# Performance work log

Hardware: AMD Instinct MI355X
Metric: run time of the kernel (lower is better)

Reference implementation:

```python
import jax, jax.numpy as jnp
import numpy as np

CHUNK = 128  # chunk size for the chunked causal linear-attention scan
EPS = 1e-6


def _feature_map(x):
    # elu(x) + 1, matching torch.nn.functional.elu (alpha=1)
    return jax.nn.elu(x) + 1.0


def _causal_linear(Q, K, V):
    """Chunked causal linear attention.

    Q, K: [N, H, L, D], V: [N, H, L, Dv] (float32).
    Computes out[l] = Q[l] @ sum_{s<=l} K[s]^T V[s] without materializing
    the O(L*D*Dv) cumulative outer-product tensor.
    """
    N, H, L, D = Q.shape
    Dv = V.shape[-1]
    C = L // CHUNK
    # [C, N, H, T, D]
    qc = jnp.moveaxis(Q.reshape(N, H, C, CHUNK, D), 2, 0)
    kc = jnp.moveaxis(K.reshape(N, H, C, CHUNK, D), 2, 0)
    vc = jnp.moveaxis(V.reshape(N, H, C, CHUNK, Dv), 2, 0)
    tri = jnp.tril(jnp.ones((CHUNK, CHUNK), dtype=Q.dtype))  # causal mask within chunk

    def step(S, qkv):
        q, k, v = qkv  # [N, H, T, D], [N, H, T, D], [N, H, T, Dv]
        attn = jnp.einsum('nhtd,nhsd->nhts', q, k) * tri
        out = jnp.einsum('nhts,nhse->nhte', attn, v) \
            + jnp.einsum('nhtd,nhde->nhte', q, S)
        S = S + jnp.einsum('nhsd,nhse->nhde', k, v)
        return S, out

    S0 = jnp.zeros((N, H, D, Dv), dtype=Q.dtype)
    _, outs = jax.lax.scan(step, S0, (qc, kc, vc))  # outs: [C, N, H, T, Dv]
    return jnp.moveaxis(outs, 0, 2).reshape(N, H, L, Dv)


def setup_inputs() -> dict:
    key = jax.random.key(0)
    kq, kk, kv = jax.random.split(key, 3)
    shape = (4, 8192, 8, 64)  # [N, L, H, D]
    return {
        'queries': jax.random.normal(kq, shape, dtype=jnp.float32),
        'keys': jax.random.normal(kk, shape, dtype=jnp.float32),
        'values': jax.random.normal(kv, shape, dtype=jnp.float32),
    }


def reference(queries, keys, values):
    dtype = queries.dtype
    Q = _feature_map(queries)  # [N, L, H, D]
    K = _feature_map(keys)
    # normalizer: Z = 1 / (Q . cumsum_l(K) + eps), shape [N, L, H]
    Z = 1.0 / (jnp.einsum('nlhi,nlhi->nlh', Q, jnp.cumsum(K, axis=1)) + EPS)
    # numerator computed in float32 per original causal_linear
    Qf = jnp.transpose(Q, (0, 2, 1, 3)).astype(jnp.float32)
    Kf = jnp.transpose(K, (0, 2, 1, 3)).astype(jnp.float32)
    Vf = jnp.transpose(values, (0, 2, 1, 3)).astype(jnp.float32)
    Vn = _causal_linear(Qf, Kf, Vf)  # [N, H, L, Dv]
    Vn = jnp.transpose(Vn, (0, 2, 1, 3)).astype(dtype)  # [N, L, H, Dv]
    return Vn * Z[:, :, :, None]
```

## Files before the change

### kernel.cpp

```cpp
#include <hip/hip_runtime.h>
#include <hip/hip_bf16.h>
#include <math.h>

#define N_    4
#define L_    8192
#define H_    8
#define NH_   32
#define CHK   64
#define NC_   128
#define ROWF  512
#define EPSF  1e-6f

typedef __attribute__((ext_vector_type(8))) short bf16x8;
typedef __attribute__((ext_vector_type(4))) float f32x4;
typedef __attribute__((ext_vector_type(4))) unsigned short us4;

__device__ __forceinline__ float fmap(float x) { return x > 0.f ? x + 1.f : __expf(x); }

__device__ __forceinline__ unsigned short c2bf(float x) {
  __hip_bfloat16 b = __float2bfloat16(x);
  return *reinterpret_cast<unsigned short*>(&b);
}
__device__ __forceinline__ float bf2f(unsigned short u) {
  return __uint_as_float(((unsigned)u) << 16);
}

__device__ __forceinline__ int sidx(int row, int col) {
  return row * 64 + (col ^ ((row & 7) << 3));
}

__device__ __forceinline__ f32x4 MFMA(bf16x8 a, bf16x8 b, f32x4 c) {
  return __builtin_amdgcn_mfma_f32_16x16x32_bf16(a, b, c, 0, 0, 0);
}

__global__ __launch_bounds__(512) void k_chunk_tot(const float* __restrict__ keys,
                                                   const float* __restrict__ values,
                                                   unsigned short* __restrict__ Tws,
                                                   float* __restrict__ Kcs) {
  __shared__ __align__(16) unsigned short Kt[64 * 64];
  __shared__ __align__(16) unsigned short Vt[64 * 64];
  __shared__ float kacc[64];
  const int bid = blockIdx.x;
  const int nh = bid / NC_, c = bid % NC_;
  const int n = nh / H_, h = nh % H_;
  const int tid = threadIdx.x;
  const int lane = tid & 63;
  const int wv = tid >> 6;
  const int lane15 = lane & 15, lg = lane >> 4;
  const int arow = (wv & 3) * 16 + lane15;
  const int nt0 = (wv >> 2) * 2;

  if (tid < 64) kacc[tid] = 0.f;

  const int d = tid & 63, sg = tid >> 6;
  const size_t gbase = ((size_t)(n * L_ + c * CHK)) * ROWF + h * 64 + d;
  float kr[8], vr[8];
#pragma unroll
  for (int i = 0; i < 8; ++i) kr[i] = keys[gbase + (size_t)(sg * 8 + i) * ROWF];
#pragma unroll
  for (int i = 0; i < 8; ++i) vr[i] = values[gbase + (size_t)(sg * 8 + i) * ROWF];
  __builtin_amdgcn_sched_barrier(0);

  float kpart = 0.f;
#pragma unroll
  for (int i = 0; i < 8; ++i) { kr[i] = fmap(kr[i]); kpart += kr[i]; }
#pragma unroll
  for (int i = 0; i < 8; i += 4) {
    us4 wk, wvv;
#pragma unroll
    for (int j = 0; j < 4; ++j) { wk[j] = c2bf(kr[i + j]); wvv[j] = c2bf(vr[i + j]); }
    *(us4*)&Kt[sidx(d, sg * 8 + i)] = wk;
    *(us4*)&Vt[sidx(d, sg * 8 + i)] = wvv;
  }
  atomicAdd(&kacc[d], kpart);
  __syncthreads();

  const bf16x8 av0 = *(const bf16x8*)&Vt[sidx(arow, lg * 8)];
  const bf16x8 av1 = *(const bf16x8*)&Vt[sidx(arow, (lg + 4) * 8)];
  unsigned short* Tp = Tws + (size_t)bid * 4096;
#pragma unroll
  for (int t2 = 0; t2 < 2; ++t2) {
    const int nt = nt0 + t2;
    const int brow = nt * 16 + lane15;
    f32x4 acc = {0.f, 0.f, 0.f, 0.f};
    acc = MFMA(*(const bf16x8*)&Kt[sidx(brow, lg * 8)], av0, acc);
    acc = MFMA(*(const bf16x8*)&Kt[sidx(brow, (lg + 4) * 8)], av1, acc);
    us4 w;
#pragma unroll
    for (int r = 0; r < 4; ++r) w[r] = c2bf(acc[r]);
    *(us4*)&Tp[sidx(arow, nt * 16 + lg * 4)] = w;
  }
  if (tid < 64) Kcs[(size_t)bid * 64 + tid] = kacc[tid];
}

__global__ __launch_bounds__(256) void k_scan(unsigned short* __restrict__ Tws,
                                              float* __restrict__ Kcs) {
  const int tid = threadIdx.x;
  if (blockIdx.x < 512) {
    const int gid = blockIdx.x * 256 + tid;
    const int nh = gid >> 12, de = gid & 4095;
    unsigned short* p = Tws + (size_t)nh * NC_ * 4096 + de;
    float run = 0.f;
    for (int s = 0; s < 32; ++s) {
      const float x0 = bf2f(p[(size_t)(s * 4 + 0) * 4096]);
      const float x1 = bf2f(p[(size_t)(s * 4 + 1) * 4096]);
      const float x2 = bf2f(p[(size_t)(s * 4 + 2) * 4096]);
      const float x3 = bf2f(p[(size_t)(s * 4 + 3) * 4096]);
      p[(size_t)(s * 4 + 0) * 4096] = c2bf(run);
      p[(size_t)(s * 4 + 1) * 4096] = c2bf(run + x0);
      p[(size_t)(s * 4 + 2) * 4096] = c2bf(run + x0 + x1);
      p[(size_t)(s * 4 + 3) * 4096] = c2bf(run + x0 + x1 + x2);
      run += x0 + x1 + x2 + x3;
    }
  } else {
    const int gid = (blockIdx.x - 512) * 256 + tid;
    const int nh = gid >> 6, d = gid & 63;
    float* p = Kcs + (size_t)nh * NC_ * 64 + d;
    float run = 0.f;
    for (int s = 0; s < 32; ++s) {
      const float x0 = p[(size_t)(s * 4 + 0) * 64];
      const float x1 = p[(size_t)(s * 4 + 1) * 64];
      const float x2 = p[(size_t)(s * 4 + 2) * 64];
      const float x3 = p[(size_t)(s * 4 + 3) * 64];
      p[(size_t)(s * 4 + 0) * 64] = run;
      p[(size_t)(s * 4 + 1) * 64] = run + x0;
      p[(size_t)(s * 4 + 2) * 64] = run + x0 + x1;
      p[(size_t)(s * 4 + 3) * 64] = run + x0 + x1 + x2;
      run += x0 + x1 + x2 + x3;
    }
  }
}

__global__ __launch_bounds__(256, 4) void k_output(const float* __restrict__ queries,
                                                   const float* __restrict__ keys,
                                                   const float* __restrict__ values,
                                                   const unsigned short* __restrict__ Pws,
                                                   const float* __restrict__ Kpre,
                                                   float* __restrict__ out) {
  __shared__ __align__(16) unsigned short Ks[64 * 64];
  __shared__ __align__(16) unsigned short Vt[64 * 64];
  __shared__ __align__(16) unsigned short St[64 * 64];

  const int wg = blockIdx.x;
  const int bid = (wg & 7) * (NH_ * NC_ / 8) + (wg >> 3);
  const int nh = bid / NC_, c = bid % NC_;
  const int n = nh / H_, h = nh % H_;
  const int tid = threadIdx.x;
  const int lane = tid & 63;
  const int wv = tid >> 6;
  const int lane15 = lane & 15, lg = lane >> 4;
  const int t0w = wv * 16;
  const int trow = t0w + lane15;
  const int l0 = c * CHK;
  const size_t tb = (size_t)bid * 4096;
  const size_t kb = (size_t)bid * 64;

  const size_t qg = ((size_t)(n * L_ + l0 + trow)) * ROWF + h * 64;
  const float4 q0 = *(const float4*)&queries[qg + lg * 8];
  const float4 q1 = *(const float4*)&queries[qg + lg * 8 + 4];
  const float4 q2 = *(const float4*)&queries[qg + 32 + lg * 8];
  const float4 q3 = *(const float4*)&queries[qg + 32 + lg * 8 + 4];
  const int r0 = tid >> 4, c4 = (tid & 15) * 4;
  float4 krow[4];
#pragma unroll
  for (int rep = 0; rep < 4; ++rep)
    krow[rep] = *(const float4*)&keys[((size_t)(n * L_ + l0 + r0 + rep * 16)) * ROWF + h * 64 + c4];
  const int d = tid & 63, sg = tid >> 6;
  const size_t vbase = ((size_t)(n * L_ + l0)) * ROWF + h * 64 + d;
  float vr[16];
#pragma unroll
  for (int i = 0; i < 16; ++i) vr[i] = values[vbase + (size_t)(sg * 16 + i) * ROWF];
  const uint4 st0 = *(const uint4*)&Pws[tb + tid * 8];
  const uint4 st1 = *(const uint4*)&Pws[tb + (tid + 256) * 8];
  const float4 kp0 = *(const float4*)&Kpre[kb + lg * 8];
  const float4 kp1 = *(const float4*)&Kpre[kb + lg * 8 + 4];
  const float4 kp2 = *(const float4*)&Kpre[kb + 32 + lg * 8];
  const float4 kp3 = *(const float4*)&Kpre[kb + 32 + lg * 8 + 4];
  __builtin_amdgcn_sched_barrier(0);

#pragma unroll
  for (int rep = 0; rep < 4; ++rep) {
    us4 uk;
    uk[0] = c2bf(fmap(krow[rep].x)); uk[1] = c2bf(fmap(krow[rep].y));
    uk[2] = c2bf(fmap(krow[rep].z)); uk[3] = c2bf(fmap(krow[rep].w));
    *(us4*)&Ks[sidx(r0 + rep * 16, c4)] = uk;
  }
#pragma unroll
  for (int i = 0; i < 16; i += 4) {
    us4 w;
#pragma unroll
    for (int j = 0; j < 4; ++j) w[j] = c2bf(vr[i + j]);
    *(us4*)&Vt[sidx(d, sg * 16 + i)] = w;
  }
  *(uint4*)&St[tid * 8] = st0;
  *(uint4*)&St[(tid + 256) * 8] = st1;
  const float4 f0 = make_float4(fmap(q0.x), fmap(q0.y), fmap(q0.z), fmap(q0.w));
  const float4 f1 = make_float4(fmap(q1.x), fmap(q1.y), fmap(q1.z), fmap(q1.w));
  const float4 f2 = make_float4(fmap(q2.x), fmap(q2.y), fmap(q2.z), fmap(q2.w));
  const float4 f3 = make_float4(fmap(q3.x), fmap(q3.y), fmap(q3.z), fmap(q3.w));
  bf16x8 qf0, qf1;
  qf0[0] = (short)c2bf(f0.x); qf0[1] = (short)c2bf(f0.y);
  qf0[2] = (short)c2bf(f0.z); qf0[3] = (short)c2bf(f0.w);
  qf0[4] = (short)c2bf(f1.x); qf0[5] = (short)c2bf(f1.y);
  qf0[6] = (short)c2bf(f1.z); qf0[7] = (short)c2bf(f1.w);
  qf1[0] = (short)c2bf(f2.x); qf1[1] = (short)c2bf(f2.y);
  qf1[2] = (short)c2bf(f2.z); qf1[3] = (short)c2bf(f2.w);
  qf1[4] = (short)c2bf(f3.x); qf1[5] = (short)c2bf(f3.y);
  qf1[6] = (short)c2bf(f3.z); qf1[7] = (short)c2bf(f3.w);
  float zp = f0.x * kp0.x + f0.y * kp0.y + f0.z * kp0.z + f0.w * kp0.w
           + f1.x * kp1.x + f1.y * kp1.y + f1.z * kp1.z + f1.w * kp1.w
           + f2.x * kp2.x + f2.y * kp2.y + f2.z * kp2.z + f2.w * kp2.w
           + f3.x * kp3.x + f3.y * kp3.y + f3.z * kp3.z + f3.w * kp3.w;
  __syncthreads();

  f32x4 aT[4];
#pragma unroll
  for (int nt = 0; nt < 4; ++nt) {
    const int srow = nt * 16 + lane15;
    f32x4 a = {0.f, 0.f, 0.f, 0.f};
    a = MFMA(*(const bf16x8*)&Ks[sidx(srow, lg * 8)], qf0, a);
    a = MFMA(*(const bf16x8*)&Ks[sidx(srow, (lg + 4) * 8)], qf1, a);
    aT[nt] = a;
  }
  __syncthreads();

  float rs = 0.f;
#pragma unroll
  for (int nt = 0; nt < 4; ++nt) {
    us4 w;
#pragma unroll
    for (int r = 0; r < 4; ++r) {
      const int sc = nt * 16 + lg * 4 + r;
      const float v = (sc <= trow) ? aT[nt][r] : 0.f;
      rs += v;
      w[r] = c2bf(v);
    }
    *(us4*)&Ks[sidx(trow, nt * 16 + lg * 4)] = w;
  }
  float den = rs + zp;
  den += __shfl_xor(den, 16);
  den += __shfl_xor(den, 32);
  const float zv = 1.f / (den + EPSF);

  const bf16x8 af0 = *(const bf16x8*)&Ks[sidx(trow, lg * 8)];
  const bf16x8 af1 = *(const bf16x8*)&Ks[sidx(trow, 32 + lg * 8)];
  const size_t obase = ((size_t)(n * L_ + l0 + trow)) * ROWF + h * 64;
#pragma unroll
  for (int nt = 0; nt < 4; ++nt) {
    const int brow = nt * 16 + lane15;
    f32x4 o = {0.f, 0.f, 0.f, 0.f};
    o = MFMA(*(const bf16x8*)&Vt[sidx(brow, lg * 8)], af0, o);
    o = MFMA(*(const bf16x8*)&Vt[sidx(brow, (lg + 4) * 8)], af1, o);
    o = MFMA(*(const bf16x8*)&St[sidx(brow, lg * 8)], qf0, o);
    o = MFMA(*(const bf16x8*)&St[sidx(brow, (lg + 4) * 8)], qf1, o);
    const float4 w = make_float4(o[0] * zv, o[1] * zv, o[2] * zv, o[3] * zv);
    *(float4*)&out[obase + nt * 16 + lg * 4] = w;
  }
}

extern "C" void kernel_launch(void* const* d_in, const int* in_sizes, int n_in,
                              void* d_out, int out_size, void* d_ws, size_t ws_size,
                              hipStream_t stream) {
  const float* queries = (const float*)d_in[0];
  const float* keys    = (const float*)d_in[1];
  const float* values  = (const float*)d_in[2];
  float* out = (float*)d_out;

  const size_t t_elems = (size_t)NH_ * NC_ * 4096;
  const size_t k_elems = (size_t)NH_ * NC_ * 64;
  if (ws_size < t_elems * 2 + k_elems * 4) return;
  unsigned short* Tws = (unsigned short*)d_ws;
  float* Kcs = (float*)(Tws + t_elems);

  hipLaunchKernelGGL(k_chunk_tot, dim3(NH_ * NC_), dim3(512), 0, stream, keys, values, Tws, Kcs);
  hipLaunchKernelGGL(k_scan, dim3(512 + 8), dim3(256), 0, stream, Tws, Kcs);
  hipLaunchKernelGGL(k_output, dim3(NH_ * NC_), dim3(256), 0, stream,
                     queries, keys, values, Tws, Kcs, out);
}
```

Baseline: 91.92 us.

## Process two chunks per workgroup in k_output, prefetching the second chunk's loads

Each k_output workgroup now handles two consecutive chunks. It issues the global loads for the second chunk into registers before computing the first chunk, so memory latency overlaps with MFMA work. The grid is halved and the launch-bounds occupancy hint drops from 4 to 3 to make room for the extra live registers. The cost is lower parallelism and occupancy, which may reduce latency hiding across waves.

```diff
diff --git a/kernel.cpp b/kernel.cpp
--- a/kernel.cpp
+++ b/kernel.cpp
@@ -131,7 +131,15 @@
   }
 }
 
-__global__ __launch_bounds__(256, 4) void k_output(const float* __restrict__ queries,
+struct CR {
+  float4 q0, q1, q2, q3;
+  float4 k0, k1, k2, k3;
+  f32x4 v0, v1, v2, v3;
+  uint4 s0, s1;
+  float4 p0, p1, p2, p3;
+};
+
+__global__ __launch_bounds__(256, 3) void k_output(const float* __restrict__ queries,
                                                    const float* __restrict__ keys,
                                                    const float* __restrict__ values,
                                                    const unsigned short* __restrict__ Pws,
@@ -142,8 +150,9 @@
   __shared__ __align__(16) unsigned short St[64 * 64];
 
   const int wg = blockIdx.x;
-  const int bid = (wg & 7) * (NH_ * NC_ / 8) + (wg >> 3);
-  const int nh = bid / NC_, c = bid % NC_;
+  const int bid2 = (wg & 7) * (NH_ * NC_ / 16) + (wg >> 3);
+  const int nh = bid2 >> 6, cp = bid2 & 63;
+  const int c0 = cp * 2, c1 = c0 + 1;
   const int n = nh / H_, h = nh % H_;
   const int tid = threadIdx.x;
   const int lane = tid & 63;
@@ -151,111 +160,146 @@
   const int lane15 = lane & 15, lg = lane >> 4;
   const int t0w = wv * 16;
   const int trow = t0w + lane15;
-  const int l0 = c * CHK;
-  const size_t tb = (size_t)bid * 4096;
-  const size_t kb = (size_t)bid * 64;
-
-  const size_t qg = ((size_t)(n * L_ + l0 + trow)) * ROWF + h * 64;
-  const float4 q0 = *(const float4*)&queries[qg + lg * 8];
-  const float4 q1 = *(const float4*)&queries[qg + lg * 8 + 4];
-  const float4 q2 = *(const float4*)&queries[qg + 32 + lg * 8];
-  const float4 q3 = *(const float4*)&queries[qg + 32 + lg * 8 + 4];
   const int r0 = tid >> 4, c4 = (tid & 15) * 4;
-  float4 krow[4];
-#pragma unroll
-  for (int rep = 0; rep < 4; ++rep)
-    krow[rep] = *(const float4*)&keys[((size_t)(n * L_ + l0 + r0 + rep * 16)) * ROWF + h * 64 + c4];
   const int d = tid & 63, sg = tid >> 6;
-  const size_t vbase = ((size_t)(n * L_ + l0)) * ROWF + h * 64 + d;
-  float vr[16];
-#pragma unroll
-  for (int i = 0; i < 16; ++i) vr[i] = values[vbase + (size_t)(sg * 16 + i) * ROWF];
-  const uint4 st0 = *(const uint4*)&Pws[tb + tid * 8];
-  const uint4 st1 = *(const uint4*)&Pws[tb + (tid + 256) * 8];
-  const float4 kp0 = *(const float4*)&Kpre[kb + lg * 8];
-  const float4 kp1 = *(const float4*)&Kpre[kb + lg * 8 + 4];
-  const float4 kp2 = *(const float4*)&Kpre[kb + 32 + lg * 8];
-  const float4 kp3 = *(const float4*)&Kpre[kb + 32 + lg * 8 + 4];
+
+  auto issue_loads = [&](int c, CR& r) {
+    const int l0 = c * CHK;
+    const size_t qg = ((size_t)(n * L_ + l0 + trow)) * ROWF + h * 64;
+    r.q0 = *(const float4*)&queries[qg + lg * 8];
+    r.q1 = *(const float4*)&queries[qg + lg * 8 + 4];
+    r.q2 = *(const float4*)&queries[qg + 32 + lg * 8];
+    r.q3 = *(const float4*)&queries[qg + 32 + lg * 8 + 4];
+    const size_t kg = ((size_t)(n * L_ + l0 + r0)) * ROWF + h * 64 + c4;
+    r.k0 = *(const float4*)&keys[kg];
+    r.k1 = *(const float4*)&keys[kg + (size_t)16 * ROWF];
+    r.k2 = *(const float4*)&keys[kg + (size_t)32 * ROWF];
+    r.k3 = *(const float4*)&keys[kg + (size_t)48 * ROWF];
+    const size_t vb = ((size_t)(n * L_ + l0)) * ROWF + h * 64 + d;
+#pragma unroll
+    for (int j = 0; j < 4; ++j) r.v0[j] = values[vb + (size_t)(sg * 16 + j) * ROWF];
+#pragma unroll
+    for (int j = 0; j < 4; ++j) r.v1[j] = values[vb + (size_t)(sg * 16 + 4 + j) * ROWF];
+#pragma unroll
+    for (int j = 0; j < 4; ++j) r.v2[j] = values[vb + (size_t)(sg * 16 + 8 + j) * ROWF];
+#pragma unroll
+    for (int j = 0; j < 4; ++j) r.v3[j] = values[vb + (size_t)(sg * 16 + 12 + j) * ROWF];
+    const size_t tb = ((size_t)nh * NC_ + c) * 4096;
+    r.s0 = *(const uint4*)&Pws[tb + tid * 8];
+    r.s1 = *(const uint4*)&Pws[tb + (tid + 256) * 8];
+    const size_t kb = ((size_t)nh * NC_ + c) * 64;
+    r.p0 = *(const float4*)&Kpre[kb + lg * 8];
+    r.p1 = *(const float4*)&Kpre[kb + lg * 8 + 4];
+    r.p2 = *(const float4*)&Kpre[kb + 32 + lg * 8];
+    r.p3 = *(const float4*)&Kpre[kb + 32 + lg * 8 + 4];
+  };
+
+  auto stage = [&](const CR& r, bf16x8& qf0, bf16x8& qf1, float& zp) {
+    us4 uk;
+    uk[0] = c2bf(fmap(r.k0.x)); uk[1] = c2bf(fmap(r.k0.y));
+    uk[2] = c2bf(fmap(r.k0.z)); uk[3] = c2bf(fmap(r.k0.w));
+    *(us4*)&Ks[sidx(r0, c4)] = uk;
+    uk[0] = c2bf(fmap(r.k1.x)); uk[1] = c2bf(fmap(r.k1.y));
+    uk[2] = c2bf(fmap(r.k1.z)); uk[3] = c2bf(fmap(r.k1.w));
+    *(us4*)&Ks[sidx(r0 + 16, c4)] = uk;
+    uk[0] = c2bf(fmap(r.k2.x)); uk[1] = c2bf(fmap(r.k2.y));
+    uk[2] = c2bf(fmap(r.k2.z)); uk[3] = c2bf(fmap(r.k2.w));
+    *(us4*)&Ks[sidx(r0 + 32, c4)] = uk;
+    uk[0] = c2bf(fmap(r.k3.x)); uk[1] = c2bf(fmap(r.k3.y));
+    uk[2] = c2bf(fmap(r.k3.z)); uk[3] = c2bf(fmap(r.k3.w));
+    *(us4*)&Ks[sidx(r0 + 48, c4)] = uk;
+    us4 w;
+    w[0] = c2bf(r.v0[0]); w[1] = c2bf(r.v0[1]); w[2] = c2bf(r.v0[2]); w[3] = c2bf(r.v0[3]);
+    *(us4*)&Vt[sidx(d, sg * 16)] = w;
+    w[0] = c2bf(r.v1[0]); w[1] = c2bf(r.v1[1]); w[2] = c2bf(r.v1[2]); w[3] = c2bf(r.v1[3]);
+    *(us4*)&Vt[sidx(d, sg * 16 + 4)] = w;
+    w[0] = c2bf(r.v2[0]); w[1] = c2bf(r.v2[1]); w[2] = c2bf(r.v2[2]); w[3] = c2bf(r.v2[3]);
+    *(us4*)&Vt[sidx(d, sg * 16 + 8)] = w;
+    w[0] = c2bf(r.v3[0]); w[1] = c2bf(r.v3[1]); w[2] = c2bf(r.v3[2]); w[3] = c2bf(r.v3[3]);
+    *(us4*)&Vt[sidx(d, sg * 16 + 12)] = w;
+    *(uint4*)&St[tid * 8] = r.s0;
+    *(uint4*)&St[(tid + 256) * 8] = r.s1;
+    const float4 f0 = make_float4(fmap(r.q0.x), fmap(r.q0.y), fmap(r.q0.z), fmap(r.q0.w));
+    const float4 f1 = make_float4(fmap(r.q1.x), fmap(r.q1.y), fmap(r.q1.z), fmap(r.q1.w));
+    const float4 f2 = make_float4(fmap(r.q2.x), fmap(r.q2.y), fmap(r.q2.z), fmap(r.q2.w));
+    const float4 f3 = make_float4(fmap(r.q3.x), fmap(r.q3.y), fmap(r.q3.z), fmap(r.q3.w));
+    qf0[0] = (short)c2bf(f0.x); qf0[1] = (short)c2bf(f0.y);
+    qf0[2] = (short)c2bf(f0.z); qf0[3] = (short)c2bf(f0.w);
+    qf0[4] = (short)c2bf(f1.x); qf0[5] = (short)c2bf(f1.y);
+    qf0[6] = (short)c2bf(f1.z); qf0[7] = (short)c2bf(f1.w);
+    qf1[0] = (short)c2bf(f2.x); qf1[1] = (short)c2bf(f2.y);
+    qf1[2] = (short)c2bf(f2.z); qf1[3] = (short)c2bf(f2.w);
+    qf1[4] = (short)c2bf(f3.x); qf1[5] = (short)c2bf(f3.y);
+    qf1[6] = (short)c2bf(f3.z); qf1[7] = (short)c2bf(f3.w);
+    zp = f0.x * r.p0.x + f0.y * r.p0.y + f0.z * r.p0.z + f0.w * r.p0.w
+       + f1.x * r.p1.x + f1.y * r.p1.y + f1.z * r.p1.z + f1.w * r.p1.w
+       + f2.x * r.p2.x + f2.y * r.p2.y + f2.z * r.p2.z + f2.w * r.p2.w
+       + f3.x * r.p3.x + f3.y * r.p3.y + f3.z * r.p3.z + f3.w * r.p3.w;
+  };
+
+  auto compute_store = [&](int c, bf16x8 qf0, bf16x8 qf1, float zp) {
+    const int l0 = c * CHK;
+    f32x4 aT[4];
+#pragma unroll
+    for (int nt = 0; nt < 4; ++nt) {
+      const int srow = nt * 16 + lane15;
+      f32x4 a = {0.f, 0.f, 0.f, 0.f};
+      a = MFMA(*(const bf16x8*)&Ks[sidx(srow, lg * 8)], qf0, a);
+      a = MFMA(*(const bf16x8*)&Ks[sidx(srow, (lg + 4) * 8)], qf1, a);
+      aT[nt] = a;
+    }
+    __syncthreads();
+
+    float rs = 0.f;
+#pragma unroll
+    for (int nt = 0; nt < 4; ++nt) {
+      us4 w;
+#pragma unroll
+      for (int r = 0; r < 4; ++r) {
+        const int sc = nt * 16 + lg * 4 + r;
+        const float v = (sc <= trow) ? aT[nt][r] : 0.f;
+        rs += v;
+        w[r] = c2bf(v);
+      }
+      *(us4*)&Ks[sidx(trow, nt * 16 + lg * 4)] = w;
+    }
+    float den = rs + zp;
+    den += __shfl_xor(den, 16);
+    den += __shfl_xor(den, 32);
+    const float zv = 1.f / (den + EPSF);
+
+    const bf16x8 af0 = *(const bf16x8*)&Ks[sidx(trow, lg * 8)];
+    const bf16x8 af1 = *(const bf16x8*)&Ks[sidx(trow, 32 + lg * 8)];
+    const size_t obase = ((size_t)(n * L_ + l0 + trow)) * ROWF + h * 64;
+#pragma unroll
+    for (int nt = 0; nt < 4; ++nt) {
+      const int brow = nt * 16 + lane15;
+      f32x4 o = {0.f, 0.f, 0.f, 0.f};
+      o = MFMA(*(const bf16x8*)&Vt[sidx(brow, lg * 8)], af0, o);
+      o = MFMA(*(const bf16x8*)&Vt[sidx(brow, (lg + 4) * 8)], af1, o);
+      o = MFMA(*(const bf16x8*)&St[sidx(brow, lg * 8)], qf0, o);
+      o = MFMA(*(const bf16x8*)&St[sidx(brow, (lg + 4) * 8)], qf1, o);
+      const float4 w = make_float4(o[0] * zv, o[1] * zv, o[2] * zv, o[3] * zv);
+      *(float4*)&out[obase + nt * 16 + lg * 4] = w;
+    }
+  };
+
+  CR rA, rB;
+  issue_loads(c0, rA);
+  bf16x8 qA0, qA1; float zpA;
+  stage(rA, qA0, qA1, zpA);
+  __syncthreads();
+
+  issue_loads(c1, rB);
   __builtin_amdgcn_sched_barrier(0);
 
-#pragma unroll
-  for (int rep = 0; rep < 4; ++rep) {
-    us4 uk;
-    uk[0] = c2bf(fmap(krow[rep].x)); uk[1] = c2bf(fmap(krow[rep].y));
-    uk[2] = c2bf(fmap(krow[rep].z)); uk[3] = c2bf(fmap(krow[rep].w));
-    *(us4*)&Ks[sidx(r0 + rep * 16, c4)] = uk;
-  }
-#pragma unroll
-  for (int i = 0; i < 16; i += 4) {
-    us4 w;
-#pragma unroll
-    for (int j = 0; j < 4; ++j) w[j] = c2bf(vr[i + j]);
-    *(us4*)&Vt[sidx(d, sg * 16 + i)] = w;
-  }
-  *(uint4*)&St[tid * 8] = st0;
-  *(uint4*)&St[(tid + 256) * 8] = st1;
-  const float4 f0 = make_float4(fmap(q0.x), fmap(q0.y), fmap(q0.z), fmap(q0.w));
-  const float4 f1 = make_float4(fmap(q1.x), fmap(q1.y), fmap(q1.z), fmap(q1.w));
-  const float4 f2 = make_float4(fmap(q2.x), fmap(q2.y), fmap(q2.z), fmap(q2.w));
-  const float4 f3 = make_float4(fmap(q3.x), fmap(q3.y), fmap(q3.z), fmap(q3.w));
-  bf16x8 qf0, qf1;
-  qf0[0] = (short)c2bf(f0.x); qf0[1] = (short)c2bf(f0.y);
-  qf0[2] = (short)c2bf(f0.z); qf0[3] = (short)c2bf(f0.w);
-  qf0[4] = (short)c2bf(f1.x); qf0[5] = (short)c2bf(f1.y);
-  qf0[6] = (short)c2bf(f1.z); qf0[7] = (short)c2bf(f1.w);
-  qf1[0] = (short)c2bf(f2.x); qf1[1] = (short)c2bf(f2.y);
-  qf1[2] = (short)c2bf(f2.z); qf1[3] = (short)c2bf(f2.w);
-  qf1[4] = (short)c2bf(f3.x); qf1[5] = (short)c2bf(f3.y);
-  qf1[6] = (short)c2bf(f3.z); qf1[7] = (short)c2bf(f3.w);
-  float zp = f0.x * kp0.x + f0.y * kp0.y + f0.z * kp0.z + f0.w * kp0.w
-           + f1.x * kp1.x + f1.y * kp1.y + f1.z * kp1.z + f1.w * kp1.w
-           + f2.x * kp2.x + f2.y * kp2.y + f2.z * kp2.z + f2.w * kp2.w
-           + f3.x * kp3.x + f3.y * kp3.y + f3.z * kp3.z + f3.w * kp3.w;
+  compute_store(c0, qA0, qA1, zpA);
   __syncthreads();
 
-  f32x4 aT[4];
-#pragma unroll
-  for (int nt = 0; nt < 4; ++nt) {
-    const int srow = nt * 16 + lane15;
-    f32x4 a = {0.f, 0.f, 0.f, 0.f};
-    a = MFMA(*(const bf16x8*)&Ks[sidx(srow, lg * 8)], qf0, a);
-    a = MFMA(*(const bf16x8*)&Ks[sidx(srow, (lg + 4) * 8)], qf1, a);
-    aT[nt] = a;
-  }
+  bf16x8 qB0, qB1; float zpB;
+  stage(rB, qB0, qB1, zpB);
   __syncthreads();
-
-  float rs = 0.f;
-#pragma unroll
-  for (int nt = 0; nt < 4; ++nt) {
-    us4 w;
-#pragma unroll
-    for (int r = 0; r < 4; ++r) {
-      const int sc = nt * 16 + lg * 4 + r;
-      const float v = (sc <= trow) ? aT[nt][r] : 0.f;
-      rs += v;
-      w[r] = c2bf(v);
-    }
-    *(us4*)&Ks[sidx(trow, nt * 16 + lg * 4)] = w;
-  }
-  float den = rs + zp;
-  den += __shfl_xor(den, 16);
-  den += __shfl_xor(den, 32);
-  const float zv = 1.f / (den + EPSF);
-
-  const bf16x8 af0 = *(const bf16x8*)&Ks[sidx(trow, lg * 8)];
-  const bf16x8 af1 = *(const bf16x8*)&Ks[sidx(trow, 32 + lg * 8)];
-  const size_t obase = ((size_t)(n * L_ + l0 + trow)) * ROWF + h * 64;
-#pragma unroll
-  for (int nt = 0; nt < 4; ++nt) {
-    const int brow = nt * 16 + lane15;
-    f32x4 o = {0.f, 0.f, 0.f, 0.f};
-    o = MFMA(*(const bf16x8*)&Vt[sidx(brow, lg * 8)], af0, o);
-    o = MFMA(*(const bf16x8*)&Vt[sidx(brow, (lg + 4) * 8)], af1, o);
-    o = MFMA(*(const bf16x8*)&St[sidx(brow, lg * 8)], qf0, o);
-    o = MFMA(*(const bf16x8*)&St[sidx(brow, (lg + 4) * 8)], qf1, o);
-    const float4 w = make_float4(o[0] * zv, o[1] * zv, o[2] * zv, o[3] * zv);
-    *(float4*)&out[obase + nt * 16 + lg * 4] = w;
-  }
+  compute_store(c1, qB0, qB1, zpB);
 }
 
 extern "C" void kernel_launch(void* const* d_in, const int* in_sizes, int n_in,
@@ -274,6 +318,6 @@
 
   hipLaunchKernelGGL(k_chunk_tot, dim3(NH_ * NC_), dim3(512), 0, stream, keys, values, Tws, Kcs);
   hipLaunchKernelGGL(k_scan, dim3(512 + 8), dim3(256), 0, stream, Tws, Kcs);
-  hipLaunchKernelGGL(k_output, dim3(NH_ * NC_), dim3(256), 0, stream,
+  hipLaunchKernelGGL(k_output, dim3(NH_ * NC_ / 2), dim3(256), 0, stream,
                      queries, keys, values, Tws, Kcs, out);
 }
```

After: 94.71 us. 3.0% more time.
